# Optimization experiments

Measured on AMD Instinct MI355X. Metric: run time of the kernel, lower is better.

Reference implementation:

```python
import jax, jax.numpy as jnp
import numpy as np

B, T, S, D, H = 2, 2048, 2048, 2048, 16
HD = D // H  # 128
SCALE = 1.0 / np.sqrt(HD)


def _rope(x, cos, sin):
    # x: [B,H,S,HD]; cos/sin: [1,1,S,HD//2]
    b, h, s, d = x.shape
    xs = x.reshape(b, h, s, d // 2, 2)
    x0, x1 = xs[..., 0], xs[..., 1]
    rot = jnp.stack([x0 * cos - x1 * sin, x1 * cos + x0 * sin], axis=-1)
    return rot.reshape(b, h, s, d)


def _split_heads(x):
    b, s, _ = x.shape
    return x.reshape(b, s, H, HD).transpose(0, 2, 1, 3)


def setup_inputs() -> dict:
    key = jax.random.key(0)
    ks = jax.random.split(key, 6)
    w_std = (1.0 / np.sqrt(2.0)) * np.sqrt(6.0 / (D + D))  # xavier_uniform with gain 1/sqrt(2)
    def xavier(k):
        return jax.random.uniform(k, (D, D), jnp.float32, -w_std, w_std)
    # rotary tables (standard inv-freq form)
    inv_freq = 1.0 / (10000.0 ** (np.arange(0, HD, 2, dtype=np.float32) / HD))  # [HD//2]
    ang = np.arange(T, dtype=np.float32)[:, None] * inv_freq[None, :]           # [T,HD//2]
    cos = jnp.asarray(np.cos(ang), jnp.float32)[None, None]  # [1,1,T,HD//2]
    sin = jnp.asarray(np.sin(ang), jnp.float32)[None, None]
    return {
        "hidden_states": jax.random.normal(ks[0], (B, T, D), jnp.float32),
        "encoder_hidden_states": jax.random.normal(ks[1], (B, S, D), jnp.float32),
        "Wq": xavier(ks[2]),
        "Wk": xavier(ks[3]),
        "Wv": xavier(ks[4]),
        "Wo": xavier(ks[5]),
        "cos_q": cos, "sin_q": sin,
        "cos_k": cos, "sin_k": sin,
    }


def reference(hidden_states, encoder_hidden_states, Wq, Wk, Wv, Wo,
              cos_q, sin_q, cos_k, sin_k):
    # Linear (no bias): y = x @ W.T
    q = _split_heads(jnp.einsum('btd,ed->bte', hidden_states, Wq))          # [B,H,T,HD]
    k = _split_heads(jnp.einsum('bsd,ed->bse', encoder_hidden_states, Wk))  # [B,H,S,HD]
    v = _split_heads(jnp.einsum('bsd,ed->bse', encoder_hidden_states, Wv))  # [B,H,S,HD]
    q = _rope(q, cos_q, sin_q)
    k = _rope(k, cos_k, sin_k)
    scores = jnp.einsum('bhtd,bhsd->bhts', q, k) * SCALE                    # [B,H,T,S]
    attn = jax.nn.softmax(scores.astype(jnp.float32), axis=-1)
    ctx = jnp.einsum('bhts,bhsd->bhtd', attn, v)                            # [B,H,T,HD]
    ctx = ctx.transpose(0, 2, 1, 3).reshape(B, T, D)                        # merge heads
    return jnp.einsum('btd,ed->bte', ctx, Wo)
```

## Files before the change

kernel.cpp:

```cpp
#include <hip/hip_runtime.h>
#include <cmath>

#define SCALE_F 0.088388347648318447f

typedef _Float16 f16;
typedef _Float16 f16x8 __attribute__((ext_vector_type(8)));
typedef _Float16 f16x4 __attribute__((ext_vector_type(4)));
typedef float f32x4 __attribute__((ext_vector_type(4)));
typedef float f32x16 __attribute__((ext_vector_type(16)));
typedef unsigned int u32;
typedef unsigned int u32x2 __attribute__((ext_vector_type(2)));
typedef unsigned int u32x4 __attribute__((ext_vector_type(4)));

#define MFMA16(a, b, c) __builtin_amdgcn_mfma_f32_16x16x32_f16(a, b, c, 0, 0, 0)
#define MFMA32(a, b, c) __builtin_amdgcn_mfma_f32_32x32x16_f16(a, b, c, 0, 0, 0)
#define Z16 ((f32x16){0.f,0.f,0.f,0.f,0.f,0.f,0.f,0.f,0.f,0.f,0.f,0.f,0.f,0.f,0.f,0.f})
#define EX2(x) __builtin_amdgcn_exp2f(x)

__device__ __forceinline__ void gl2lds16(const f16* g, f16* l) {
    __builtin_amdgcn_global_load_lds(
        (const __attribute__((address_space(1))) unsigned int*)g,
        (__attribute__((address_space(3))) unsigned int*)l, 16, 0, 0);
}

__device__ __forceinline__ u32 pk2(float x, float y) {
    const unsigned short a = __builtin_bit_cast(unsigned short, (f16)x);
    const unsigned short b = __builtin_bit_cast(unsigned short, (f16)y);
    return (u32)a | ((u32)b << 16);
}
__device__ __forceinline__ float fswapsum(float x) {
    u32 a = __builtin_bit_cast(u32, x), b;
    asm volatile("v_mov_b32 %0, %1" : "=&v"(b) : "v"(a));
    asm volatile("v_permlane32_swap_b32 %0, %1" : "+v"(a), "+v"(b));
    return __builtin_bit_cast(float, a) + __builtin_bit_cast(float, b);
}
__device__ __forceinline__ float fswapmax(float x) {
    u32 a = __builtin_bit_cast(u32, x), b;
    asm volatile("v_mov_b32 %0, %1" : "=&v"(b) : "v"(a));
    asm volatile("v_permlane32_swap_b32 %0, %1" : "+v"(a), "+v"(b));
    return fmaxf(__builtin_bit_cast(float, a), __builtin_bit_cast(float, b));
}

__global__ __launch_bounds__(256) void cvt_all(
    const float* __restrict__ hs, const float* __restrict__ es,
    const float* __restrict__ Wq, const float* __restrict__ Wk,
    const float* __restrict__ Wv, const float* __restrict__ Wo,
    f16* __restrict__ dst)
{
    const int c = blockIdx.x * 256 + threadIdx.x;
    const float* src; int off;
    if (c < 2097152) { src = (c < 1048576) ? hs : es; off = c & 1048575; }
    else {
        const int cc = c - 2097152;
        const int wsel = cc >> 19; off = cc & 524287;
        src = wsel == 0 ? Wq : wsel == 1 ? Wk : wsel == 2 ? Wv : Wo;
    }
    const float4* p = (const float4*)src + (size_t)off * 2;
    const float4 a = p[0], b2 = p[1];
    f16x8 o = {(f16)a.x, (f16)a.y, (f16)a.z, (f16)a.w,
               (f16)b2.x, (f16)b2.y, (f16)b2.z, (f16)b2.w};
    *(f16x8*)(dst + (size_t)c * 8) = o;
}

template <int OUT_MODE>
__global__ __launch_bounds__(256, 2) void gemm16(
    const f16* __restrict__ A, const f16* __restrict__ W,
    void* __restrict__ Cv, int M, int N, int K,
    const float* __restrict__ Cs, const float* __restrict__ Sn)
{
    __shared__ __align__(16) f16 Al[128 * 64];
    __shared__ __align__(16) f16 Bl[128 * 64];
    const int tid = threadIdx.x;
    const int l = tid & 63, w = tid >> 6;
    const int wr = w >> 1, wc = w & 1;

    const int nwg = gridDim.x, cpx = nwg >> 3;
    const int bid = blockIdx.x;
    const int swz = (bid & 7) * cpx + (bid >> 3);
    const int nbn = N >> 7;
    const int bm = (swz / nbn) * 128, bn = (swz % nbn) * 128;

    f32x4 acc[4][4];
#pragma unroll
    for (int i = 0; i < 4; ++i)
#pragma unroll
        for (int j = 0; j < 4; ++j) acc[i][j] = (f32x4){0.f, 0.f, 0.f, 0.f};

    const int srow = tid >> 3;
    const int sg = tid & 7;

    for (int k0 = 0; k0 < K; k0 += 64) {
        __syncthreads();
#pragma unroll
        for (int i = 0; i < 4; ++i) {
            const int row = i * 32 + srow;
            const int lg = sg ^ (row & 7);
            gl2lds16(A + (size_t)(bm + row) * K + k0 + lg * 8, Al + row * 64 + sg * 8);
            gl2lds16(W + (size_t)(bn + row) * K + k0 + lg * 8, Bl + row * 64 + sg * 8);
        }
        __syncthreads();
#pragma unroll
        for (int kk = 0; kk < 2; ++kk) {
            f16x8 a[4], b[4];
            const int g = kk * 4 + (l >> 4);
#pragma unroll
            for (int m = 0; m < 4; ++m) {
                const int row = wr * 64 + m * 16 + (l & 15);
                a[m] = *(const f16x8*)(Al + row * 64 + (g ^ (row & 7)) * 8);
            }
#pragma unroll
            for (int n = 0; n < 4; ++n) {
                const int row = wc * 64 + n * 16 + (l & 15);
                b[n] = *(const f16x8*)(Bl + row * 64 + (g ^ (row & 7)) * 8);
            }
#pragma unroll
            for (int m = 0; m < 4; ++m)
#pragma unroll
                for (int n = 0; n < 4; ++n)
                    acc[m][n] = MFMA16(a[m], b[n], acc[m][n]);
        }
    }

#pragma unroll
    for (int m = 0; m < 4; ++m)
#pragma unroll
        for (int n = 0; n < 4; ++n)
#pragma unroll
            for (int j = 0; j < 4; ++j) {
                const int r = bm + wr * 64 + m * 16 + ((l >> 4) << 2) + j;
                const int c = bn + wc * 64 + n * 16 + (l & 15);
                if (OUT_MODE == 0) {
                    ((f16*)Cv)[(size_t)r * N + c] = (f16)acc[m][n][j];
                } else if (OUT_MODE == 2) {
                    ((float*)Cv)[(size_t)r * N + c] = acc[m][n][j];
                } else if (OUT_MODE == 3) {
                    ((f16*)Cv)[(size_t)((c >> 11) * 2048 + r) * 2048 + (c & 2047)] = (f16)acc[m][n][j];
                } else if (OUT_MODE == 4) {
                    const float v = acc[m][n][j];
                    const float vp = __shfl_xor(v, 1);
                    const int t = r & 2047;
                    const int i2 = (c & 127) >> 1;
                    const float co = Cs[t * 64 + i2];
                    const float si = Sn[t * 64 + i2];
                    const float y = (c & 1) ? fmaf(v, co, vp * si) : fmaf(v, co, -vp * si);
                    ((f16*)Cv)[(size_t)r * N + c] = (f16)y;
                }
            }
}

__global__ __launch_bounds__(256, 2) void attn16(
    const f16* __restrict__ Qg, const f16* __restrict__ Kg,
    const f16* __restrict__ Vt, f16* __restrict__ Og)
{
    __shared__ __align__(16) f16 Kl[2][64 * 132];
    __shared__ __align__(16) f16 Vl[2][128 * 68];
    __shared__ float bnc[4][32];

    const int tid = threadIdx.x;
    const int l = tid & 63, w = tid >> 6;
    const int l31 = l & 31, hi = l >> 5;
    const int hi4 = hi * 4;

    const int krow = tid >> 4, kg = tid & 15;
    const int vd = tid >> 3, vg = tid & 7;

    const int bid = blockIdx.x;
    const int swz = (bid & 7) * 64 + (bid >> 3);
    const int bh = swz >> 4, qt = swz & 15;
    const int b = bh >> 4, h = bh & 15;

    const int qrow = b * 2048 + qt * 128 + w * 32 + l31;
    const f16 qsc = (f16)(0.088388347648318447f * 1.44269504088896f);
    f16x8 qf[8];
#pragma unroll
    for (int kc = 0; kc < 8; ++kc) {
        f16x8 t0 = *(const f16x8*)(Qg + (size_t)qrow * 2048 + h * 128 + kc * 16 + hi * 8);
#pragma unroll
        for (int e = 0; e < 8; ++e) t0[e] = t0[e] * qsc;
        qf[kc] = t0;
    }

    f32x16 o[4] = {Z16, Z16, Z16, Z16};
    float mrow = -3.0e38f, lrow = 0.0f;

    const f16* Kbase = Kg + (size_t)(b * 2048) * 2048 + h * 128;
    const f16* Vbase = Vt + (size_t)(b * 2048 + h * 128) * 2048;

    u32x4 kst[4], vst[4];

#define LOADT(st) do {                                                                   \
    _Pragma("unroll")                                                                    \
    for (int u = 0; u < 4; ++u)                                                          \
        kst[u] = *(const u32x4*)(Kbase + (size_t)((st) + krow + u * 16) * 2048 + kg * 8);\
    _Pragma("unroll")                                                                    \
    for (int u = 0; u < 4; ++u)                                                          \
        vst[u] = *(const u32x4*)(Vbase + (size_t)(vd + u * 32) * 2048 + (st) + vg * 8);  \
} while (0)

#define WRITET(bf) do {                                                                  \
    _Pragma("unroll")                                                                    \
    for (int u = 0; u < 4; ++u) {                                                        \
        f16* p = &Kl[bf][(krow + u * 16) * 132 + kg * 8];                                \
        *(u32x2*)p       = (u32x2){kst[u].x, kst[u].y};                                  \
        *(u32x2*)(p + 4) = (u32x2){kst[u].z, kst[u].w};                                  \
    }                                                                                    \
    _Pragma("unroll")                                                                    \
    for (int u = 0; u < 4; ++u) {                                                        \
        f16* p = &Vl[bf][(vd + u * 32) * 68 + vg * 8];                                   \
        *(u32x2*)p       = (u32x2){vst[u].x, vst[u].y};                                  \
        *(u32x2*)(p + 4) = (u32x2){vst[u].z, vst[u].w};                                  \
    }                                                                                    \
} while (0)

    LOADT(0);
    WRITET(0);
    __syncthreads();

    int cur = 0;
    for (int t = 0; t < 32; ++t) {
        if (t < 31) LOADT((t + 1) * 64);
        const f16* Kc = Kl[cur];
        const f16* Vc = Vl[cur];

        f32x16 p0 = Z16, p1 = Z16;
        __builtin_amdgcn_s_setprio(1);
#pragma unroll
        for (int kc = 0; kc < 8; ++kc) {
            const int go = (kc * 2 + hi) * 8;
            const f16* kp0 = Kc + l31 * 132 + go;
            const f16* kp1 = Kc + (32 + l31) * 132 + go;
            const f16x4 a0 = *(const f16x4*)kp0, a1 = *(const f16x4*)(kp0 + 4);
            const f16x4 b0 = *(const f16x4*)kp1, b1 = *(const f16x4*)(kp1 + 4);
            const f16x8 k0 = __builtin_shufflevector(a0, a1, 0, 1, 2, 3, 4, 5, 6, 7);
            const f16x8 k1 = __builtin_shufflevector(b0, b1, 0, 1, 2, 3, 4, 5, 6, 7);
            p0 = MFMA32(k0, qf[kc], p0);
            p1 = MFMA32(k1, qf[kc], p1);
        }
        __builtin_amdgcn_s_setprio(0);

        float mt[16];
#pragma unroll
        for (int r = 0; r < 16; ++r) mt[r] = fmaxf(p0[r], p1[r]);
#pragma unroll
        for (int r = 0; r < 8; ++r) mt[r] = fmaxf(mt[r], mt[r + 8]);
#pragma unroll
        for (int r = 0; r < 4; ++r) mt[r] = fmaxf(mt[r], mt[r + 4]);
        float mx = fmaxf(fmaxf(mt[0], mt[1]), fmaxf(mt[2], mt[3]));
        mx = fswapmax(mx);

        if (!__all(mx <= mrow + 8.0f)) {
            const float mn = fmaxf(mrow, mx);
            const float cr = EX2(mrow - mn);
            mrow = mn;
            lrow *= cr;
            if (hi == 0) bnc[w][l31] = cr;
#pragma unroll
            for (int r = 0; r < 16; ++r) {
                const float crr = bnc[w][(r & 3) + 8 * (r >> 2) + 4 * hi];
                o[0][r] *= crr; o[1][r] *= crr; o[2][r] *= crr; o[3][r] *= crr;
            }
        }

        float st16[16];
#pragma unroll
        for (int r = 0; r < 16; ++r) {
            p0[r] = EX2(p0[r] - mrow);
            p1[r] = EX2(p1[r] - mrow);
            st16[r] = p0[r] + p1[r];
        }
#pragma unroll
        for (int r = 0; r < 8; ++r) st16[r] += st16[r + 8];
#pragma unroll
        for (int r = 0; r < 4; ++r) st16[r] += st16[r + 4];
        lrow += fswapsum((st16[0] + st16[1]) + (st16[2] + st16[3]));

        f16x8 pf[4];
#pragma unroll
        for (int ksl = 0; ksl < 2; ++ksl) {
            u32x4 w0 = {pk2(p0[8*ksl+0], p0[8*ksl+1]), pk2(p0[8*ksl+2], p0[8*ksl+3]),
                        pk2(p0[8*ksl+4], p0[8*ksl+5]), pk2(p0[8*ksl+6], p0[8*ksl+7])};
            pf[ksl] = __builtin_bit_cast(f16x8, w0);
            u32x4 w1 = {pk2(p1[8*ksl+0], p1[8*ksl+1]), pk2(p1[8*ksl+2], p1[8*ksl+3]),
                        pk2(p1[8*ksl+4], p1[8*ksl+5]), pk2(p1[8*ksl+6], p1[8*ksl+7])};
            pf[2 + ksl] = __builtin_bit_cast(f16x8, w1);
        }

        if (t < 31) WRITET(cur ^ 1);

        __builtin_amdgcn_s_setprio(1);
#pragma unroll
        for (int dt = 0; dt < 4; ++dt) {
            const f16* vrow = Vc + (dt * 32 + l31) * 68;
#pragma unroll
            for (int ks = 0; ks < 4; ++ks) {
                const f16x4 vlo = *(const f16x4*)(vrow + ks * 16 + hi4);
                const f16x4 vhi = *(const f16x4*)(vrow + ks * 16 + hi4 + 8);
                const f16x8 vf = __builtin_shufflevector(vlo, vhi, 0, 1, 2, 3, 4, 5, 6, 7);
                o[dt] = MFMA32(pf[ks], vf, o[dt]);
            }
        }
        __builtin_amdgcn_s_setprio(0);

        __syncthreads();
        cur ^= 1;
    }
#undef LOADT
#undef WRITET

    const float inv = 1.0f / lrow;
    if (hi == 0) bnc[w][l31] = inv;
#pragma unroll
    for (int r = 0; r < 16; ++r) {
        const int qq = (r & 3) + 8 * (r >> 2) + 4 * hi;
        const float ir = bnc[w][qq];
        const size_t row = (size_t)(b * 2048 + qt * 128 + w * 32 + qq);
#pragma unroll
        for (int dt = 0; dt < 4; ++dt)
            Og[row * 2048 + h * 128 + dt * 32 + l31] = (f16)(o[dt][r] * ir);
    }
}

extern "C" void kernel_launch(void* const* d_in, const int* in_sizes, int n_in,
                              void* d_out, int out_size, void* d_ws, size_t ws_size,
                              hipStream_t stream) {
    const float* hs = (const float*)d_in[0];
    const float* es = (const float*)d_in[1];
    const float* Wq = (const float*)d_in[2];
    const float* Wk = (const float*)d_in[3];
    const float* Wv = (const float*)d_in[4];
    const float* Wo = (const float*)d_in[5];
    const float* cq = (const float*)d_in[6];
    const float* sq = (const float*)d_in[7];
    const float* ck = (const float*)d_in[8];
    const float* sk = (const float*)d_in[9];
    float* out = (float*)d_out;

    f16* hs16 = (f16*)d_ws;
    f16* es16 = hs16 + 8388608;
    f16* Wq16 = es16 + 8388608;
    f16* Wk16 = Wq16 + 4194304;
    f16* Wv16 = Wk16 + 4194304;
    f16* Wo16 = Wv16 + 4194304;
    f16* Q16  = Wo16 + 4194304;
    f16* K16  = Q16 + 8388608;
    f16* Vt16 = K16 + 8388608;
    f16* ctx16 = hs16;

    const dim3 tB(256);
    cvt_all<<<dim3(16384), tB, 0, stream>>>(hs, es, Wq, Wk, Wv, Wo, hs16);

    gemm16<4><<<dim3(512), tB, 0, stream>>>(hs16, Wq16, Q16, 4096, 2048, 2048, cq, sq);
    gemm16<4><<<dim3(512), tB, 0, stream>>>(es16, Wk16, K16, 4096, 2048, 2048, ck, sk);
    gemm16<3><<<dim3(512), tB, 0, stream>>>(Wv16, es16, Vt16, 2048, 4096, 2048, nullptr, nullptr);

    attn16<<<dim3(512), tB, 0, stream>>>(Q16, K16, Vt16, ctx16);

    gemm16<2><<<dim3(512), tB, 0, stream>>>(ctx16, Wo16, out, 4096, 2048, 2048, nullptr, nullptr);
}
```

Baseline: 290.1 us.

## Single-buffer attention LDS to allow four blocks per CU, use pkrtz and max3

```diff
diff --git a/kernel.cpp b/kernel.cpp
--- a/kernel.cpp
+++ b/kernel.cpp
@@ -6,6 +6,7 @@
 typedef _Float16 f16;
 typedef _Float16 f16x8 __attribute__((ext_vector_type(8)));
 typedef _Float16 f16x4 __attribute__((ext_vector_type(4)));
+typedef __fp16 fp16x2 __attribute__((ext_vector_type(2)));
 typedef float f32x4 __attribute__((ext_vector_type(4)));
 typedef float f32x16 __attribute__((ext_vector_type(16)));
 typedef unsigned int u32;
@@ -23,10 +24,9 @@
         (__attribute__((address_space(3))) unsigned int*)l, 16, 0, 0);
 }
 
-__device__ __forceinline__ u32 pk2(float x, float y) {
-    const unsigned short a = __builtin_bit_cast(unsigned short, (f16)x);
-    const unsigned short b = __builtin_bit_cast(unsigned short, (f16)y);
-    return (u32)a | ((u32)b << 16);
+__device__ __forceinline__ u32 pkz(float x, float y) {
+    fp16x2 h = __builtin_amdgcn_cvt_pkrtz(x, y);
+    return __builtin_bit_cast(u32, h);
 }
 __device__ __forceinline__ float fswapsum(float x) {
     u32 a = __builtin_bit_cast(u32, x), b;
@@ -40,6 +40,7 @@
     asm volatile("v_permlane32_swap_b32 %0, %1" : "+v"(a), "+v"(b));
     return fmaxf(__builtin_bit_cast(float, a), __builtin_bit_cast(float, b));
 }
+#define MAX3(a, b, c) fmaxf(fmaxf((a), (b)), (c))
 
 __global__ __launch_bounds__(256) void cvt_all(
     const float* __restrict__ hs, const float* __restrict__ es,
@@ -148,12 +149,12 @@
             }
 }
 
-__global__ __launch_bounds__(256, 2) void attn16(
+__global__ __launch_bounds__(256, 4) void attn16(
     const f16* __restrict__ Qg, const f16* __restrict__ Kg,
     const f16* __restrict__ Vt, f16* __restrict__ Og)
 {
-    __shared__ __align__(16) f16 Kl[2][64 * 132];
-    __shared__ __align__(16) f16 Vl[2][128 * 68];
+    __shared__ __align__(16) f16 Kl[64 * 132];
+    __shared__ __align__(16) f16 Vl[128 * 68];
     __shared__ float bnc[4][32];
 
     const int tid = threadIdx.x;
@@ -197,38 +198,35 @@
         vst[u] = *(const u32x4*)(Vbase + (size_t)(vd + u * 32) * 2048 + (st) + vg * 8);  \
 } while (0)
 
-#define WRITET(bf) do {                                                                  \
+#define WRITET() do {                                                                    \
     _Pragma("unroll")                                                                    \
     for (int u = 0; u < 4; ++u) {                                                        \
-        f16* p = &Kl[bf][(krow + u * 16) * 132 + kg * 8];                                \
+        f16* p = &Kl[(krow + u * 16) * 132 + kg * 8];                                    \
         *(u32x2*)p       = (u32x2){kst[u].x, kst[u].y};                                  \
         *(u32x2*)(p + 4) = (u32x2){kst[u].z, kst[u].w};                                  \
     }                                                                                    \
     _Pragma("unroll")                                                                    \
     for (int u = 0; u < 4; ++u) {                                                        \
-        f16* p = &Vl[bf][(vd + u * 32) * 68 + vg * 8];                                   \
+        f16* p = &Vl[(vd + u * 32) * 68 + vg * 8];                                       \
         *(u32x2*)p       = (u32x2){vst[u].x, vst[u].y};                                  \
         *(u32x2*)(p + 4) = (u32x2){vst[u].z, vst[u].w};                                  \
     }                                                                                    \
 } while (0)
 
     LOADT(0);
-    WRITET(0);
+    WRITET();
     __syncthreads();
 
-    int cur = 0;
     for (int t = 0; t < 32; ++t) {
         if (t < 31) LOADT((t + 1) * 64);
-        const f16* Kc = Kl[cur];
-        const f16* Vc = Vl[cur];
 
         f32x16 p0 = Z16, p1 = Z16;
         __builtin_amdgcn_s_setprio(1);
 #pragma unroll
         for (int kc = 0; kc < 8; ++kc) {
             const int go = (kc * 2 + hi) * 8;
-            const f16* kp0 = Kc + l31 * 132 + go;
-            const f16* kp1 = Kc + (32 + l31) * 132 + go;
+            const f16* kp0 = Kl + l31 * 132 + go;
+            const f16* kp1 = Kl + (32 + l31) * 132 + go;
             const f16x4 a0 = *(const f16x4*)kp0, a1 = *(const f16x4*)(kp0 + 4);
             const f16x4 b0 = *(const f16x4*)kp1, b1 = *(const f16x4*)(kp1 + 4);
             const f16x8 k0 = __builtin_shufflevector(a0, a1, 0, 1, 2, 3, 4, 5, 6, 7);
@@ -238,14 +236,18 @@
         }
         __builtin_amdgcn_s_setprio(0);
 
-        float mt[16];
-#pragma unroll
-        for (int r = 0; r < 16; ++r) mt[r] = fmaxf(p0[r], p1[r]);
-#pragma unroll
-        for (int r = 0; r < 8; ++r) mt[r] = fmaxf(mt[r], mt[r + 8]);
-#pragma unroll
-        for (int r = 0; r < 4; ++r) mt[r] = fmaxf(mt[r], mt[r + 4]);
-        float mx = fmaxf(fmaxf(mt[0], mt[1]), fmaxf(mt[2], mt[3]));
+        float pp[32];
+#pragma unroll
+        for (int r = 0; r < 16; ++r) { pp[r] = p0[r]; pp[16 + r] = p1[r]; }
+        float mv[11];
+#pragma unroll
+        for (int i = 0; i < 10; ++i) mv[i] = MAX3(pp[3 * i], pp[3 * i + 1], pp[3 * i + 2]);
+        mv[10] = fmaxf(pp[30], pp[31]);
+        const float n0 = MAX3(mv[0], mv[1], mv[2]);
+        const float n1 = MAX3(mv[3], mv[4], mv[5]);
+        const float n2 = MAX3(mv[6], mv[7], mv[8]);
+        const float n3 = MAX3(mv[9], mv[10], n0);
+        float mx = MAX3(n1, n2, n3);
         mx = fswapmax(mx);
 
         if (!__all(mx <= mrow + 8.0f)) {
@@ -277,20 +279,18 @@
         f16x8 pf[4];
 #pragma unroll
         for (int ksl = 0; ksl < 2; ++ksl) {
-            u32x4 w0 = {pk2(p0[8*ksl+0], p0[8*ksl+1]), pk2(p0[8*ksl+2], p0[8*ksl+3]),
-                        pk2(p0[8*ksl+4], p0[8*ksl+5]), pk2(p0[8*ksl+6], p0[8*ksl+7])};
+            u32x4 w0 = {pkz(p0[8*ksl+0], p0[8*ksl+1]), pkz(p0[8*ksl+2], p0[8*ksl+3]),
+                        pkz(p0[8*ksl+4], p0[8*ksl+5]), pkz(p0[8*ksl+6], p0[8*ksl+7])};
             pf[ksl] = __builtin_bit_cast(f16x8, w0);
-            u32x4 w1 = {pk2(p1[8*ksl+0], p1[8*ksl+1]), pk2(p1[8*ksl+2], p1[8*ksl+3]),
-                        pk2(p1[8*ksl+4], p1[8*ksl+5]), pk2(p1[8*ksl+6], p1[8*ksl+7])};
+            u32x4 w1 = {pkz(p1[8*ksl+0], p1[8*ksl+1]), pkz(p1[8*ksl+2], p1[8*ksl+3]),
+                        pkz(p1[8*ksl+4], p1[8*ksl+5]), pkz(p1[8*ksl+6], p1[8*ksl+7])};
             pf[2 + ksl] = __builtin_bit_cast(f16x8, w1);
         }
 
-        if (t < 31) WRITET(cur ^ 1);
-
         __builtin_amdgcn_s_setprio(1);
 #pragma unroll
         for (int dt = 0; dt < 4; ++dt) {
-            const f16* vrow = Vc + (dt * 32 + l31) * 68;
+            const f16* vrow = Vl + (dt * 32 + l31) * 68;
 #pragma unroll
             for (int ks = 0; ks < 4; ++ks) {
                 const f16x4 vlo = *(const f16x4*)(vrow + ks * 16 + hi4);
@@ -302,7 +302,10 @@
         __builtin_amdgcn_s_setprio(0);
 
         __syncthreads();
-        cur ^= 1;
+        if (t < 31) {
+            WRITET();
+            __syncthreads();
+        }
     }
 #undef LOADT
 #undef WRITET
```

After: 449.5 us. 55.0% more time.
